# Performance work log

Measured on AMD Instinct MI355X. Metric: run time of the kernel, lower is better.

## Reference

```python
import jax, jax.numpy as jnp
import numpy as np
from jax import lax

H = 128


def _lstm_dir(x, Wih, Whh, bih, bhh):
    # Single-direction LSTM, PyTorch gate order (i, f, g, o).
    # x: [B, L, D]; Wih: [4H, D]; Whh: [4H, H]; bih/bhh: [4H]
    B, L, _ = x.shape
    Hs = Whh.shape[1]
    # Precompute input contributions for all timesteps: [B, L, 4H]
    xg = jnp.einsum('bld,gd->blg', x, Wih) + bih + bhh

    def step(carry, g_t):
        h, c = carry
        g = g_t + h @ Whh.T
        i, f, gg, o = jnp.split(g, 4, axis=-1)
        c = jax.nn.sigmoid(f) * c + jax.nn.sigmoid(i) * jnp.tanh(gg)
        h = jax.nn.sigmoid(o) * jnp.tanh(c)
        return (h, c), h

    h0 = jnp.zeros((B, Hs), x.dtype)
    _, ys = lax.scan(step, (h0, h0), jnp.swapaxes(xg, 0, 1))  # [L, B, H]
    return jnp.swapaxes(ys, 0, 1)


def _bilstm(x, Wih, Whh, bih, bhh):
    # Wih: [2, 4H, D] (dir 0 = forward, dir 1 = backward)
    yf = _lstm_dir(x, Wih[0], Whh[0], bih[0], bhh[0])
    yb = _lstm_dir(x[:, ::-1], Wih[1], Whh[1], bih[1], bhh[1])[:, ::-1]
    return jnp.concatenate([yf, yb], axis=-1)


def _lstm_params(key, din):
    ks = jax.random.split(key, 4)
    s = 1.0 / np.sqrt(H)
    u = lambda k, shp: jax.random.uniform(k, shp, jnp.float32, -s, s)
    return (u(ks[0], (2, 4 * H, din)), u(ks[1], (2, 4 * H, H)),
            u(ks[2], (2, 4 * H)), u(ks[3], (2, 4 * H)))


def setup_inputs() -> dict:
    key = jax.random.key(0)
    ks = jax.random.split(key, 8)
    B, L, D, OUT = 128, 512, 13, 2
    inp = {'x': jax.random.normal(ks[0], (B, L, D), jnp.float32)}
    for name, din, k in [('1', D, ks[1]), ('21', 2 * H, ks[2]), ('22', D, ks[3]),
                         ('31', 4 * H, ks[4]), ('32', 2 * H, ks[5])]:
        Wih, Whh, bih, bhh = _lstm_params(k, din)
        inp['Wih' + name] = Wih
        inp['Whh' + name] = Whh
        inp['bih' + name] = bih
        inp['bhh' + name] = bhh
    s4 = 1.0 / np.sqrt(4 * H)
    sf = 1.0 / np.sqrt(H)
    k4 = jax.random.split(ks[6], 2)
    kf = jax.random.split(ks[7], 2)
    inp['l4_w'] = jax.random.uniform(k4[0], (H, 4 * H), jnp.float32, -s4, s4)
    inp['l4_b'] = jax.random.uniform(k4[1], (H,), jnp.float32, -s4, s4)
    inp['fc_w'] = jax.random.uniform(kf[0], (OUT, H), jnp.float32, -sf, sf)
    inp['fc_b'] = jax.random.uniform(kf[1], (OUT,), jnp.float32, -sf, sf)
    return inp


def reference(x, Wih1, Whh1, bih1, bhh1, Wih21, Whh21, bih21, bhh21,
              Wih22, Whh22, bih22, bhh22, Wih31, Whh31, bih31, bhh31,
              Wih32, Whh32, bih32, bhh32, l4_w, l4_b, fc_w, fc_b):
    y1 = _bilstm(x, Wih1, Whh1, bih1, bhh1)              # [B, L, 2H]
    y21 = _bilstm(y1, Wih21, Whh21, bih21, bhh21)        # [B, L, 2H]
    y22 = _bilstm(x, Wih22, Whh22, bih22, bhh22)         # [B, L, 2H]
    y2 = jnp.concatenate([y21, y22], axis=2)             # [B, L, 4H]
    y31 = _bilstm(y2, Wih31, Whh31, bih31, bhh31)        # [B, L, 2H]
    y32 = _bilstm(y21, Wih32, Whh32, bih32, bhh32)       # [B, L, 2H]
    y3 = jnp.max(jnp.concatenate([y31, y32], axis=2), axis=1)  # [B, 4H]
    y4 = jax.nn.selu(y3 @ l4_w.T + l4_b)                 # dropout is identity at eval
    return jax.nn.sigmoid(y4 @ fc_w.T + fc_b)            # [B, 2]
```

## Files before the change

### kernel.cpp

```cpp
#include <hip/hip_runtime.h>
#include <hip/hip_bf16.h>

typedef __attribute__((ext_vector_type(8))) short bf16x8;
typedef __attribute__((ext_vector_type(4))) float f32x4;
typedef __attribute__((ext_vector_type(2))) _Float16 f16x2;

__device__ __forceinline__ float bfbits(unsigned short u) {
  return __uint_as_float(((unsigned int)u) << 16);
}
__device__ __forceinline__ float rcpf(float x) { return __builtin_amdgcn_rcpf(x); }
__device__ __forceinline__ float sigf(float x) { return rcpf(1.f + __expf(-x)); }
__device__ __forceinline__ float tanhf_(float x) {
  x = fminf(15.f, fmaxf(-15.f, x));
  float t = __expf(2.f * x);
  return 1.f - 2.f * rcpf(t + 1.f);
}
#if __has_builtin(__builtin_amdgcn_fdot2)
__device__ __forceinline__ float FDOT2(f16x2 a, f16x2 b, float c) {
  return __builtin_amdgcn_fdot2(a, b, c, false);
}
#else
__device__ __forceinline__ float FDOT2(f16x2 a, f16x2 b, float c) {
  return c + (float)a.x * (float)b.x + (float)a.y * (float)b.y;
}
#endif
__device__ __forceinline__ f16x2 h2bc(unsigned int u) {
  return __builtin_bit_cast(f16x2, u);
}
__device__ __forceinline__ unsigned packh(float a, float b) {
  _Float16 ha = (_Float16)a, hb = (_Float16)b;
  return (unsigned)__builtin_bit_cast(unsigned short, ha) |
         ((unsigned)__builtin_bit_cast(unsigned short, hb) << 16);
}

__global__ __launch_bounds__(256) void wconv(
    const float* whh0, const float* whh1, const float* whh2, const float* whh3, const float* whh4,
    const float* wi21, const float* wi31, const float* wi32,
    const float* bi0, const float* bh0, const float* bi1, const float* bh1,
    const float* bi2, const float* bh2, const float* bi3, const float* bh3,
    const float* bi4, const float* bh4,
    float* whht, __hip_bfloat16* wihbf, float* bsum)
{
  int tid = blockIdx.x * 256 + threadIdx.x;
  if (tid < 5 * 131072) {
    int lay = tid / 131072, r = tid % 131072;
    const float* src = lay == 0 ? whh0 : lay == 1 ? whh1 : lay == 2 ? whh2 : lay == 3 ? whh3 : whh4;
    int d = r >> 16;
    int k = (r >> 9) & 127;
    int j = r & 511;
    whht[tid] = src[((size_t)d * 512 + j) * 128 + k];
    return;
  }
  int t2 = tid - 5 * 131072;
  if (t2 < 1048576) {
    const float* src; int idx;
    if (t2 < 262144)      { src = wi21; idx = t2; }
    else if (t2 < 786432) { src = wi31; idx = t2 - 262144; }
    else                  { src = wi32; idx = t2 - 786432; }
    wihbf[t2] = __float2bfloat16(src[idx]);
    return;
  }
  int t3 = t2 - 1048576;
  if (t3 < 5120) {
    int lay = t3 >> 10, idx = t3 & 1023;
    const float* bi = lay == 0 ? bi0 : lay == 1 ? bi1 : lay == 2 ? bi2 : lay == 3 ? bi3 : bi4;
    const float* bh = lay == 0 ? bh0 : lay == 1 ? bh1 : lay == 2 ? bh2 : lay == 3 ? bh3 : bh4;
    bsum[t3] = bi[idx] + bh[idx];
  }
}

__global__ __launch_bounds__(256) void projM(
    const __hip_bfloat16* __restrict__ A, int lda, int K,
    const __hip_bfloat16* __restrict__ Bw,
    const float* __restrict__ bsum,
    __hip_bfloat16* __restrict__ out)
{
  int d = blockIdx.z;
  const __hip_bfloat16* Bp = Bw + (size_t)d * 512 * K;
  const float* bs = bsum + d * 512;
  __hip_bfloat16* op = out + (size_t)d * 65536 * 512;
  int m0 = blockIdx.y * 128, n0 = blockIdx.x * 128;
  __shared__ __align__(16) __hip_bfloat16 As[128][32];
  __shared__ __align__(16) __hip_bfloat16 Bs[128][32];
  int tid = threadIdx.x, w = tid >> 6, l = tid & 63;
  int wm = (w >> 1) * 64, wn = (w & 1) * 64;
  f32x4 acc[4][4];
#pragma unroll
  for (int mi = 0; mi < 4; ++mi)
#pragma unroll
    for (int ni = 0; ni < 4; ++ni) acc[mi][ni] = (f32x4){0.f, 0.f, 0.f, 0.f};
  int srow = tid >> 2, sc = tid & 3;
  for (int k0 = 0; k0 < K; k0 += 32) {
#pragma unroll
    for (int p = 0; p < 2; ++p) {
      int row = p * 64 + srow;
      int slot = sc ^ (row & 3);
      uint4 va = *(const uint4*)(A + (size_t)(m0 + row) * lda + k0 + sc * 8);
      *(uint4*)(&As[row][slot * 8]) = va;
      uint4 vb = *(const uint4*)(Bp + (size_t)(n0 + row) * K + k0 + sc * 8);
      *(uint4*)(&Bs[row][slot * 8]) = vb;
    }
    __syncthreads();
    bf16x8 af[4], bfr[4];
#pragma unroll
    for (int mi = 0; mi < 4; ++mi) {
      int row = wm + mi * 16 + (l & 15);
      int slot = (l >> 4) ^ (row & 3);
      af[mi] = *(const bf16x8*)(&As[row][slot * 8]);
    }
#pragma unroll
    for (int ni = 0; ni < 4; ++ni) {
      int row = wn + ni * 16 + (l & 15);
      int slot = (l >> 4) ^ (row & 3);
      bfr[ni] = *(const bf16x8*)(&Bs[row][slot * 8]);
    }
#pragma unroll
    for (int mi = 0; mi < 4; ++mi)
#pragma unroll
      for (int ni = 0; ni < 4; ++ni)
        acc[mi][ni] = __builtin_amdgcn_mfma_f32_16x16x32_bf16(af[mi], bfr[ni], acc[mi][ni], 0, 0, 0);
    __syncthreads();
  }
#pragma unroll
  for (int ni = 0; ni < 4; ++ni) {
    int col = n0 + wn + ni * 16 + (l & 15);
    float bsv = bs[col];
#pragma unroll
    for (int mi = 0; mi < 4; ++mi) {
#pragma unroll
      for (int q = 0; q < 4; ++q) {
        int row = m0 + wm + mi * 16 + (l >> 4) * 4 + q;
        op[(size_t)row * 512 + col] = __float2bfloat16(acc[mi][ni][q] + bsv);
      }
    }
  }
}

struct ScanP {
  const __hip_bfloat16* xg;
  const float* wihx;
  const float* bs;
  const float* whht;
  __hip_bfloat16* yout; int ycols; int ycoloff;
  float* y3out; int y3off;
};

#define DOT32(W, HL, curx, S0, S1) { \
  const uint4* hb4_ = (const uint4*)&HL[curx][kq * 16]; \
  uint4 hA_ = hb4_[0], hB_ = hb4_[1]; \
  float a00_ = 0.f, a01_ = 0.f, a10_ = 0.f, a11_ = 0.f; \
  unsigned int u0_[8] = {hA_.x, hA_.y, hA_.z, hA_.w, hB_.x, hB_.y, hB_.z, hB_.w}; \
  _Pragma("unroll") \
  for (int m = 0; m < 8; m += 2) { \
    f16x2 h0_ = h2bc(u0_[m]), h1_ = h2bc(u0_[m + 1]); \
    a00_ = FDOT2(W[m], h0_, a00_);           a01_ = FDOT2(W[m + 1], h1_, a01_); \
    a10_ = FDOT2(W[16 + m], h0_, a10_);      a11_ = FDOT2(W[16 + m + 1], h1_, a11_); } \
  uint4 hC_ = hb4_[2], hD_ = hb4_[3]; \
  unsigned int u1_[8] = {hC_.x, hC_.y, hC_.z, hC_.w, hD_.x, hD_.y, hD_.z, hD_.w}; \
  _Pragma("unroll") \
  for (int m = 0; m < 8; m += 2) { \
    f16x2 h0_ = h2bc(u1_[m]), h1_ = h2bc(u1_[m + 1]); \
    a00_ = FDOT2(W[8 + m], h0_, a00_);       a01_ = FDOT2(W[8 + m + 1], h1_, a01_); \
    a10_ = FDOT2(W[24 + m], h0_, a10_);      a11_ = FDOT2(W[24 + m + 1], h1_, a11_); } \
  S0 = a00_ + a01_; S1 = a10_ + a11_; }

#define CELLPHASE(P, CT, PL, HL, CURX, TROW) { \
  int ct_ = (CT); \
  float gi = PL[0][ct_] + PL[1][ct_] + PL[2][ct_] + PL[3][ct_]; \
  float gf = PL[0][ct_ + 128] + PL[1][ct_ + 128] + PL[2][ct_ + 128] + PL[3][ct_ + 128]; \
  float gg = PL[0][ct_ + 256] + PL[1][ct_ + 256] + PL[2][ct_ + 256] + PL[3][ct_ + 256]; \
  float go = PL[0][ct_ + 384] + PL[1][ct_ + 384] + PL[2][ct_ + 384] + PL[3][ct_ + 384]; \
  creg = sigf(gf) * creg + sigf(gi) * tanhf_(gg); \
  float h_ = sigf(go) * tanhf_(creg); \
  _Float16 hf_ = (_Float16)h_; \
  ((unsigned short*)&HL[CURX][0])[ct_] = __builtin_bit_cast(unsigned short, hf_); \
  if (P.yout) P.yout[((size_t)b * 512 + (TROW)) * P.ycols + P.ycoloff + d * 128 + ct_] = __float2bfloat16(h_); \
  else mreg = fmaxf(mreg, h_); }

template<bool DUALB, bool FUSE>
__global__ __launch_bounds__(1024, 4) void scan7(ScanP pa, ScanP pb, const float* xin)
{
  const int b = blockIdx.x, d = blockIdx.y;
  const int tid = threadIdx.x;
  const int kq = tid >> 8, j2 = tid & 255;
  __shared__ unsigned int hA[2][64];
  __shared__ unsigned int hB[DUALB ? 2 : 1][64];
  __shared__ float pA[4][512];
  __shared__ float pB[DUALB ? 4 : 1][512];
  __shared__ unsigned int x_lds[FUSE ? 4096 : 4];

  f16x2 w16A[32], w16B[DUALB ? 32 : 1];
  {
    const float* wp = pa.whht + (size_t)d * 65536;
#pragma unroll
    for (int g2 = 0; g2 < 2; ++g2)
#pragma unroll
      for (int m = 0; m < 16; ++m) {
        int k = kq * 32 + 2 * m;
        int col = j2 + g2 * 256;
        f16x2 t;
        t.x = (_Float16)wp[(size_t)k * 512 + col];
        t.y = (_Float16)wp[(size_t)(k + 1) * 512 + col];
        w16A[g2 * 16 + m] = t;
      }
  }
  if (DUALB) {
    const float* wp = pb.whht + (size_t)d * 65536;
#pragma unroll
    for (int g2 = 0; g2 < 2; ++g2)
#pragma unroll
      for (int m = 0; m < 16; ++m) {
        int k = kq * 32 + 2 * m;
        int col = j2 + g2 * 256;
        f16x2 t;
        t.x = (_Float16)wp[(size_t)k * 512 + col];
        t.y = (_Float16)wp[(size_t)(k + 1) * 512 + col];
        w16B[g2 * 16 + m] = t;
      }
  }
#pragma unroll
  for (int i = 0; i < 32; ++i) asm volatile("" : "+v"(w16A[i]));
  if (DUALB) {
#pragma unroll
    for (int i = 0; i < 32; ++i) asm volatile("" : "+v"(w16B[i]));
  }

  f16x2 wxA[4], wxB[4];
  if (FUSE) {
    int kd = kq * 4;
#pragma unroll
    for (int g2 = 0; g2 < 2; ++g2) {
      int col = j2 + g2 * 256;
#pragma unroll
      for (int p = 0; p < 2; ++p) {
        int d0 = kd + 2 * p, d1 = kd + 2 * p + 1;
        float a0 = d0 < 13 ? pa.wihx[((size_t)d * 512 + col) * 13 + d0] : (d0 == 15 ? pa.bs[d * 512 + col] : 0.f);
        float a1 = d1 < 13 ? pa.wihx[((size_t)d * 512 + col) * 13 + d1] : (d1 == 15 ? pa.bs[d * 512 + col] : 0.f);
        f16x2 ta; ta.x = (_Float16)a0; ta.y = (_Float16)a1;
        wxA[g2 * 2 + p] = ta;
        float b0 = d0 < 13 ? pb.wihx[((size_t)d * 512 + col) * 13 + d0] : (d0 == 15 ? pb.bs[d * 512 + col] : 0.f);
        float b1 = d1 < 13 ? pb.wihx[((size_t)d * 512 + col) * 13 + d1] : (d1 == 15 ? pb.bs[d * 512 + col] : 0.f);
        f16x2 tb; tb.x = (_Float16)b0; tb.y = (_Float16)b1;
        wxB[g2 * 2 + p] = tb;
      }
    }
#pragma unroll
    for (int i = 0; i < 4; ++i) { asm volatile("" : "+v"(wxA[i])); asm volatile("" : "+v"(wxB[i])); }
    for (int i = tid; i < 4096; i += 1024) {
      int t_ = i >> 3, k_ = i & 7;
      int d0 = 2 * k_, d1 = 2 * k_ + 1;
      float v0 = d0 < 13 ? xin[((size_t)b * 512 + t_) * 13 + d0] : (d0 == 15 ? 1.f : 0.f);
      float v1 = d1 < 13 ? xin[((size_t)b * 512 + t_) * 13 + d1] : (d1 == 15 ? 1.f : 0.f);
      x_lds[i] = packh(v0, v1);
    }
  }

  const unsigned short* xga = FUSE ? (const unsigned short*)0
                                   : (const unsigned short*)pa.xg + ((size_t)(d * 128 + b)) * 262144;
  const unsigned short* xgb = (DUALB && !FUSE) ? (const unsigned short*)pb.xg + ((size_t)(d * 128 + b)) * 262144
                                               : (const unsigned short*)0;

  if (tid < 64) { hA[0][tid] = 0u; if (DUALB) hB[0][tid] = 0u; }
  float creg = 0.f, mreg = -1e30f;
  int curA = 0, curB = 0;
  int tt0 = d ? 511 : 0;
  unsigned short pfa0 = 0, pfa1 = 0, pfb0 = 0, pfb1 = 0;
  if (!FUSE && kq == 0) {
    pfa0 = xga[(size_t)tt0 * 512 + j2];
    pfa1 = xga[(size_t)tt0 * 512 + j2 + 256];
    if (DUALB) {
      pfb0 = xgb[(size_t)tt0 * 512 + j2];
      pfb1 = xgb[(size_t)tt0 * 512 + j2 + 256];
    }
  }
  __syncthreads();

  for (int t = 0; t < 512; ++t) {
    int tt = d ? 511 - t : t;
    int tn = (t + 1 < 512) ? t + 1 : 511;
    int ttn = d ? 511 - tn : tn;

    unsigned short pna0 = 0, pna1 = 0;
    if (!FUSE && kq == 0) {
      pna0 = xga[(size_t)ttn * 512 + j2];
      pna1 = xga[(size_t)ttn * 512 + j2 + 256];
    }
    {
      float s0, s1;
      DOT32(w16A, hA, curA, s0, s1);
      if (FUSE) {
        uint2 xv = *(const uint2*)&x_lds[tt * 8 + kq * 2];
        f16x2 x0 = h2bc(xv.x), x1 = h2bc(xv.y);
        s0 = FDOT2(wxA[0], x0, s0); s0 = FDOT2(wxA[1], x1, s0);
        s1 = FDOT2(wxA[2], x0, s1); s1 = FDOT2(wxA[3], x1, s1);
      } else if (kq == 0) {
        s0 += bfbits(pfa0); s1 += bfbits(pfa1);
      }
      pA[kq][j2] = s0;
      pA[kq][j2 + 256] = s1;
    }
    if (DUALB && t > 0 && tid >= 128 && tid < 256) {
      int ttpB = d ? 512 - t : t - 1;
      CELLPHASE(pb, tid - 128, pB, hB, curB ^ 1, ttpB);
    }
    __syncthreads();
    if (DUALB && t > 0) curB ^= 1;

    unsigned short pnb0 = 0, pnb1 = 0;
    if (DUALB) {
      if (!FUSE && kq == 0) {
        pnb0 = xgb[(size_t)ttn * 512 + j2];
        pnb1 = xgb[(size_t)ttn * 512 + j2 + 256];
      }
      float s0, s1;
      DOT32(w16B, hB, curB, s0, s1);
      if (FUSE) {
        uint2 xv = *(const uint2*)&x_lds[tt * 8 + kq * 2];
        f16x2 x0 = h2bc(xv.x), x1 = h2bc(xv.y);
        s0 = FDOT2(wxB[0], x0, s0); s0 = FDOT2(wxB[1], x1, s0);
        s1 = FDOT2(wxB[2], x0, s1); s1 = FDOT2(wxB[3], x1, s1);
      } else if (kq == 0) {
        s0 += bfbits(pfb0); s1 += bfbits(pfb1);
      }
      pB[kq][j2] = s0;
      pB[kq][j2 + 256] = s1;
    }
    if (tid < 128) {
      CELLPHASE(pa, tid, pA, hA, curA ^ 1, tt);
    }
    __syncthreads();
    curA ^= 1;
    pfa0 = pna0; pfa1 = pna1; pfb0 = pnb0; pfb1 = pnb1;
  }
  if (DUALB && tid >= 128 && tid < 256) {
    int ttpB = d ? 0 : 511;
    CELLPHASE(pb, tid - 128, pB, hB, curB ^ 1, ttpB);
  }
  if (!pa.yout && tid < 128)
    pa.y3out[(size_t)b * 512 + pa.y3off + d * 128 + tid] = mreg;
  if (DUALB && !pb.yout && tid >= 128 && tid < 256)
    pb.y3out[(size_t)b * 512 + pb.y3off + d * 128 + (tid - 128)] = mreg;
}

__global__ __launch_bounds__(256) void head(
    const float* __restrict__ y3, const float* __restrict__ l4w,
    const float* __restrict__ l4b, const float* __restrict__ fcw,
    const float* __restrict__ fcb, float* __restrict__ outp)
{
  int b = blockIdx.x, t = threadIdx.x;
  __shared__ float row[512];
  __shared__ float y4[128];
  row[t] = y3[(size_t)b * 512 + t];
  row[t + 256] = y3[(size_t)b * 512 + t + 256];
  __syncthreads();
  if (t < 128) {
    float acc = l4b[t];
    const float* wr = l4w + (size_t)t * 512;
    for (int k = 0; k < 512; ++k) acc += row[k] * wr[k];
    const float scale = 1.0507009873554804934193349852946f;
    const float alpha = 1.6732632423543772848170429916717f;
    y4[t] = acc > 0.f ? scale * acc : scale * alpha * (__expf(acc) - 1.f);
  }
  __syncthreads();
  if (t < 2) {
    float acc = fcb[t];
    const float* wr = fcw + (size_t)t * 128;
    for (int k = 0; k < 128; ++k) acc += y4[k] * wr[k];
    outp[b * 2 + t] = 1.f / (1.f + __expf(-acc));
  }
}

extern "C" void kernel_launch(void* const* d_in, const int* in_sizes, int n_in,
                              void* d_out, int out_size, void* d_ws, size_t ws_size,
                              hipStream_t stream) {
  (void)in_sizes; (void)n_in; (void)out_size;
  const float* x     = (const float*)d_in[0];
  const float* Wih1  = (const float*)d_in[1];
  const float* Whh1  = (const float*)d_in[2];
  const float* bih1  = (const float*)d_in[3];
  const float* bhh1  = (const float*)d_in[4];
  const float* Wih21 = (const float*)d_in[5];
  const float* Whh21 = (const float*)d_in[6];
  const float* bih21 = (const float*)d_in[7];
  const float* bhh21 = (const float*)d_in[8];
  const float* Wih22 = (const float*)d_in[9];
  const float* Whh22 = (const float*)d_in[10];
  const float* bih22 = (const float*)d_in[11];
  const float* bhh22 = (const float*)d_in[12];
  const float* Wih31 = (const float*)d_in[13];
  const float* Whh31 = (const float*)d_in[14];
  const float* bih31 = (const float*)d_in[15];
  const float* bhh31 = (const float*)d_in[16];
  const float* Wih32 = (const float*)d_in[17];
  const float* Whh32 = (const float*)d_in[18];
  const float* bih32 = (const float*)d_in[19];
  const float* bhh32 = (const float*)d_in[20];
  const float* l4w   = (const float*)d_in[21];
  const float* l4b   = (const float*)d_in[22];
  const float* fcw   = (const float*)d_in[23];
  const float* fcb   = (const float*)d_in[24];

  char* ws = (char*)d_ws;
  const size_t NEED_F31 = 340545536ull;
  bool f31 = (ws_size >= NEED_F31);

  __hip_bfloat16 *xgA, *xgB, *y1, *y2, *wihbf;
  float *y3, *bsum, *whht;
  if (f31) {
    xgA   = (__hip_bfloat16*)(ws);
    xgB   = (__hip_bfloat16*)(ws + 134217728);
    y1    = (__hip_bfloat16*)(ws + 134217728);
    y2    = (__hip_bfloat16*)(ws + 268435456);
    y3    = (float*)(ws + 335544320);
    wihbf = (__hip_bfloat16*)(ws + 335806464);
    bsum  = (float*)(ws + 337903616);
    whht  = (float*)(ws + 337924096);
  } else {
    xgA   = (__hip_bfloat16*)(ws);
    xgB   = xgA;
    y1    = (__hip_bfloat16*)(ws + 134217728);
    y2    = (__hip_bfloat16*)(ws + 167772160);
    y3    = (float*)(ws + 234881024);
    wihbf = (__hip_bfloat16*)(ws + 235143168);
    bsum  = (float*)(ws + 237240320);
    whht  = (float*)(ws + 237260800);
  }

  wconv<<<6676, 256, 0, stream>>>(Whh1, Whh21, Whh22, Whh31, Whh32,
                                  Wih21, Wih31, Wih32,
                                  bih1, bhh1, bih21, bhh21, bih22, bhh22,
                                  bih31, bhh31, bih32, bhh32,
                                  whht, wihbf, bsum);

  ScanP P1  = {nullptr, Wih1,  bsum + 0 * 1024, whht + 0 * 131072, y1, 256, 0,   nullptr, 0};
  ScanP P22 = {nullptr, Wih22, bsum + 2 * 1024, whht + 2 * 131072, y2, 512, 256, nullptr, 0};
  ScanP P21 = {xgA, nullptr, nullptr, whht + 1 * 131072, y2, 512, 0, nullptr, 0};
  ScanP P31 = {xgA, nullptr, nullptr, whht + 3 * 131072, nullptr, 0, 0, y3, 0};
  ScanP P32 = {xgB, nullptr, nullptr, whht + 4 * 131072, nullptr, 0, 0, y3, 256};

  scan7<true, true><<<dim3(128, 2), 1024, 0, stream>>>(P1, P22, x);
  projM<<<dim3(4, 512, 2), 256, 0, stream>>>(y1, 256, 256, wihbf + 0, bsum + 1 * 1024, xgA);
  scan7<false, false><<<dim3(128, 2), 1024, 0, stream>>>(P21, P21, nullptr);
  if (f31) {
    projM<<<dim3(4, 512, 2), 256, 0, stream>>>(y2, 512, 512, wihbf + 262144, bsum + 3 * 1024, xgA);
    projM<<<dim3(4, 512, 2), 256, 0, stream>>>(y2, 512, 256, wihbf + 786432, bsum + 4 * 1024, xgB);
    scan7<true, false><<<dim3(128, 2), 1024, 0, stream>>>(P31, P32, nullptr);
  } else {
    projM<<<dim3(4, 512, 2), 256, 0, stream>>>(y2, 512, 512, wihbf + 262144, bsum + 3 * 1024, xgA);
    scan7<false, false><<<dim3(128, 2), 1024, 0, stream>>>(P31, P31, nullptr);
    projM<<<dim3(4, 512, 2), 256, 0, stream>>>(y2, 512, 256, wihbf + 786432, bsum + 4 * 1024, xgA);
    scan7<false, false><<<dim3(128, 2), 1024, 0, stream>>>(P32, P32, nullptr);
  }
  head<<<128, 256, 0, stream>>>(y3, l4w, l4b, fcw, fcb, (float*)d_out);
}
```

Baseline: 1.878 ms.

## Stage precomputed gates in LDS in 8-step chunks and batch y stores

```diff
diff --git a/kernel.cpp b/kernel.cpp
--- a/kernel.cpp
+++ b/kernel.cpp
@@ -164,30 +164,56 @@
     a10_ = FDOT2(W[24 + m], h0_, a10_);      a11_ = FDOT2(W[24 + m + 1], h1_, a11_); } \
   S0 = a00_ + a01_; S1 = a10_ + a11_; }
 
-#define CELLPHASE(P, CT, PL, HL, CURX, TROW) { \
-  int ct_ = (CT); \
+#define CELLPHASE(P, CT, PL, HL, CURX, TS, XS, YST) { \
+  int ct_ = (CT); int ts_ = (TS); \
   float gi = PL[0][ct_] + PL[1][ct_] + PL[2][ct_] + PL[3][ct_]; \
   float gf = PL[0][ct_ + 128] + PL[1][ct_ + 128] + PL[2][ct_ + 128] + PL[3][ct_ + 128]; \
   float gg = PL[0][ct_ + 256] + PL[1][ct_ + 256] + PL[2][ct_ + 256] + PL[3][ct_ + 256]; \
   float go = PL[0][ct_ + 384] + PL[1][ct_ + 384] + PL[2][ct_ + 384] + PL[3][ct_ + 384]; \
+  if (!FUSE) { \
+    int bs_ = (((ts_ >> 3) & 1) * 8 + (d ? (7 - (ts_ & 7)) : (ts_ & 7))) * 512; \
+    gi += bfbits(XS[bs_ + ct_]);       gf += bfbits(XS[bs_ + 128 + ct_]); \
+    gg += bfbits(XS[bs_ + 256 + ct_]); go += bfbits(XS[bs_ + 384 + ct_]); \
+  } \
   creg = sigf(gf) * creg + sigf(gi) * tanhf_(gg); \
   float h_ = sigf(go) * tanhf_(creg); \
   _Float16 hf_ = (_Float16)h_; \
   ((unsigned short*)&HL[CURX][0])[ct_] = __builtin_bit_cast(unsigned short, hf_); \
-  if (P.yout) P.yout[((size_t)b * 512 + (TROW)) * P.ycols + P.ycoloff + d * 128 + ct_] = __float2bfloat16(h_); \
-  else mreg = fmaxf(mreg, h_); }
+  if (P.yout) { \
+    __hip_bfloat16 hb_ = __float2bfloat16(h_); \
+    YST[(ts_ & 15) * 128 + ct_] = __builtin_bit_cast(unsigned short, hb_); \
+  } else mreg = fmaxf(mreg, h_); }
+
+#define YFLUSH(FC) { \
+  int fc_ = (FC); \
+  if ((half == 0 && pa.yout) || (half == 1 && DUALB && pb.yout)) { \
+    __hip_bfloat16* yp_ = half ? pb.yout : pa.yout; \
+    int yc_ = half ? pb.ycols : pa.ycols; \
+    int yo_ = half ? pb.ycoloff : pa.ycoloff; \
+    const unsigned short* ys_ = half ? ystB : ystA; \
+    int r_ = li >> 6, cw_ = li & 63; \
+    int ts_ = fc_ * 8 + r_; \
+    int tt_ = d ? 511 - ts_ : ts_; \
+    unsigned v_ = *(const unsigned*)(ys_ + ((fc_ & 1) * 8 + r_) * 128 + cw_ * 2); \
+    *(unsigned*)((unsigned short*)yp_ + ((size_t)b * 512 + tt_) * yc_ + yo_ + d * 128 + cw_ * 2) = v_; \
+  } }
 
 template<bool DUALB, bool FUSE>
-__global__ __launch_bounds__(1024, 4) void scan7(ScanP pa, ScanP pb, const float* xin)
+__global__ __launch_bounds__(1024, 4) void scan9(ScanP pa, ScanP pb, const float* xin)
 {
   const int b = blockIdx.x, d = blockIdx.y;
   const int tid = threadIdx.x;
   const int kq = tid >> 8, j2 = tid & 255;
+  const int half = tid >> 9, li = tid & 511;
   __shared__ unsigned int hA[2][64];
   __shared__ unsigned int hB[DUALB ? 2 : 1][64];
   __shared__ float pA[4][512];
   __shared__ float pB[DUALB ? 4 : 1][512];
   __shared__ unsigned int x_lds[FUSE ? 4096 : 4];
+  __shared__ __align__(16) unsigned short xsA[FUSE ? 8 : 8192];
+  __shared__ __align__(16) unsigned short xsB[(DUALB && !FUSE) ? 8192 : 8];
+  __shared__ __align__(8) unsigned short ystA[2048];
+  __shared__ __align__(8) unsigned short ystB[DUALB ? 2048 : 8];
 
   f16x2 w16A[32], w16B[DUALB ? 32 : 1];
   {
@@ -260,82 +286,75 @@
   const unsigned short* xgb = (DUALB && !FUSE) ? (const unsigned short*)pb.xg + ((size_t)(d * 128 + b)) * 262144
                                                : (const unsigned short*)0;
 
+  if (!FUSE && (half == 0 || DUALB)) {
+    int gr0 = d ? 504 : 0;
+    const unsigned short* src = half ? xgb : xga;
+    unsigned short* dstp = half ? xsB : xsA;
+    uint4 v = *(const uint4*)(src + (size_t)gr0 * 512 + li * 8);
+    *(uint4*)(dstp + li * 8) = v;
+  }
   if (tid < 64) { hA[0][tid] = 0u; if (DUALB) hB[0][tid] = 0u; }
   float creg = 0.f, mreg = -1e30f;
   int curA = 0, curB = 0;
-  int tt0 = d ? 511 : 0;
-  unsigned short pfa0 = 0, pfa1 = 0, pfb0 = 0, pfb1 = 0;
-  if (!FUSE && kq == 0) {
-    pfa0 = xga[(size_t)tt0 * 512 + j2];
-    pfa1 = xga[(size_t)tt0 * 512 + j2 + 256];
-    if (DUALB) {
-      pfb0 = xgb[(size_t)tt0 * 512 + j2];
-      pfb1 = xgb[(size_t)tt0 * 512 + j2 + 256];
-    }
-  }
   __syncthreads();
 
   for (int t = 0; t < 512; ++t) {
-    int tt = d ? 511 - t : t;
-    int tn = (t + 1 < 512) ? t + 1 : 511;
-    int ttn = d ? 511 - tn : tn;
-
-    unsigned short pna0 = 0, pna1 = 0;
-    if (!FUSE && kq == 0) {
-      pna0 = xga[(size_t)ttn * 512 + j2];
-      pna1 = xga[(size_t)ttn * 512 + j2 + 256];
-    }
+    uint4 pref; bool dopref = false;
+    if (!FUSE && (t & 7) == 0 && t + 8 < 512 && (half == 0 || DUALB)) {
+      dopref = true;
+      int grb = d ? (496 - t) : (t + 8);
+      const unsigned short* src = half ? xgb : xga;
+      pref = *(const uint4*)(src + (size_t)grb * 512 + li * 8);
+    }
+
     {
       float s0, s1;
       DOT32(w16A, hA, curA, s0, s1);
       if (FUSE) {
+        int tt = d ? 511 - t : t;
         uint2 xv = *(const uint2*)&x_lds[tt * 8 + kq * 2];
         f16x2 x0 = h2bc(xv.x), x1 = h2bc(xv.y);
         s0 = FDOT2(wxA[0], x0, s0); s0 = FDOT2(wxA[1], x1, s0);
         s1 = FDOT2(wxA[2], x0, s1); s1 = FDOT2(wxA[3], x1, s1);
-      } else if (kq == 0) {
-        s0 += bfbits(pfa0); s1 += bfbits(pfa1);
       }
       pA[kq][j2] = s0;
       pA[kq][j2 + 256] = s1;
     }
     if (DUALB && t > 0 && tid >= 128 && tid < 256) {
-      int ttpB = d ? 512 - t : t - 1;
-      CELLPHASE(pb, tid - 128, pB, hB, curB ^ 1, ttpB);
-    }
+      CELLPHASE(pb, tid - 128, pB, hB, curB ^ 1, t - 1, xsB, ystB);
+    }
+    if ((t & 7) == 1 && t >= 9) { YFLUSH((t >> 3) - 1); }
     __syncthreads();
     if (DUALB && t > 0) curB ^= 1;
 
-    unsigned short pnb0 = 0, pnb1 = 0;
     if (DUALB) {
-      if (!FUSE && kq == 0) {
-        pnb0 = xgb[(size_t)ttn * 512 + j2];
-        pnb1 = xgb[(size_t)ttn * 512 + j2 + 256];
-      }
       float s0, s1;
       DOT32(w16B, hB, curB, s0, s1);
       if (FUSE) {
+        int tt = d ? 511 - t : t;
         uint2 xv = *(const uint2*)&x_lds[tt * 8 + kq * 2];
         f16x2 x0 = h2bc(xv.x), x1 = h2bc(xv.y);
         s0 = FDOT2(wxB[0], x0, s0); s0 = FDOT2(wxB[1], x1, s0);
         s1 = FDOT2(wxB[2], x0, s1); s1 = FDOT2(wxB[3], x1, s1);
-      } else if (kq == 0) {
-        s0 += bfbits(pfb0); s1 += bfbits(pfb1);
       }
       pB[kq][j2] = s0;
       pB[kq][j2 + 256] = s1;
     }
     if (tid < 128) {
-      CELLPHASE(pa, tid, pA, hA, curA ^ 1, tt);
+      CELLPHASE(pa, tid, pA, hA, curA ^ 1, t, xsA, ystA);
+    }
+    if (dopref) {
+      unsigned short* dstp = half ? xsB : xsA;
+      *(uint4*)(dstp + ((((t >> 3) + 1) & 1) ? 4096 : 0) + li * 8) = pref;
     }
     __syncthreads();
     curA ^= 1;
-    pfa0 = pna0; pfa1 = pna1; pfb0 = pnb0; pfb1 = pnb1;
   }
   if (DUALB && tid >= 128 && tid < 256) {
-    int ttpB = d ? 0 : 511;
-    CELLPHASE(pb, tid - 128, pB, hB, curB ^ 1, ttpB);
-  }
+    CELLPHASE(pb, tid - 128, pB, hB, curB ^ 1, 511, xsB, ystB);
+  }
+  __syncthreads();
+  YFLUSH(63);
   if (!pa.yout && tid < 128)
     pa.y3out[(size_t)b * 512 + pa.y3off + d * 128 + tid] = mreg;
   if (DUALB && !pb.yout && tid >= 128 && tid < 256)
@@ -438,18 +457,18 @@
   ScanP P31 = {xgA, nullptr, nullptr, whht + 3 * 131072, nullptr, 0, 0, y3, 0};
   ScanP P32 = {xgB, nullptr, nullptr, whht + 4 * 131072, nullptr, 0, 0, y3, 256};
 
-  scan7<true, true><<<dim3(128, 2), 1024, 0, stream>>>(P1, P22, x);
+  scan9<true, true><<<dim3(128, 2), 1024, 0, stream>>>(P1, P22, x);
   projM<<<dim3(4, 512, 2), 256, 0, stream>>>(y1, 256, 256, wihbf + 0, bsum + 1 * 1024, xgA);
-  scan7<false, false><<<dim3(128, 2), 1024, 0, stream>>>(P21, P21, nullptr);
+  scan9<false, false><<<dim3(128, 2), 1024, 0, stream>>>(P21, P21, nullptr);
   if (f31) {
     projM<<<dim3(4, 512, 2), 256, 0, stream>>>(y2, 512, 512, wihbf + 262144, bsum + 3 * 1024, xgA);
     projM<<<dim3(4, 512, 2), 256, 0, stream>>>(y2, 512, 256, wihbf + 786432, bsum + 4 * 1024, xgB);
-    scan7<true, false><<<dim3(128, 2), 1024, 0, stream>>>(P31, P32, nullptr);
+    scan9<true, false><<<dim3(128, 2), 1024, 0, stream>>>(P31, P32, nullptr);
   } else {
     projM<<<dim3(4, 512, 2), 256, 0, stream>>>(y2, 512, 512, wihbf + 262144, bsum + 3 * 1024, xgA);
-    scan7<false, false><<<dim3(128, 2), 1024, 0, stream>>>(P31, P31, nullptr);
+    scan9<false, false><<<dim3(128, 2), 1024, 0, stream>>>(P31, P31, nullptr);
     projM<<<dim3(4, 512, 2), 256, 0, stream>>>(y2, 512, 256, wihbf + 786432, bsum + 4 * 1024, xgA);
-    scan7<false, false><<<dim3(128, 2), 1024, 0, stream>>>(P32, P32, nullptr);
+    scan9<false, false><<<dim3(128, 2), 1024, 0, stream>>>(P32, P32, nullptr);
   }
   head<<<128, 256, 0, stream>>>(y3, l4w, l4b, fcw, fcb, (float*)d_out);
 }
```

Result: slower. 1.922 ms (+2.3%).
